# Optimization experiments

Hardware: AMD Instinct MI355X
Metric: run time of the kernel (lower is better)

Reference implementation:

```python
import jax, jax.numpy as jnp
import numpy as np

N_ATOMS = 100000
N_BONDS = 200000
MAX_NB = 6
ATOM_FDIM = 133
BOND_FDIM = 147
HIDDEN = 300
DEPTH = 3
N_MOLS = 4000


def setup_inputs() -> dict:
    key = jax.random.key(0)
    ks = jax.random.split(key, 10)
    f_atoms = jax.random.normal(ks[0], (N_ATOMS, ATOM_FDIM), dtype=jnp.float32)
    f_bonds = jax.random.normal(ks[1], (N_BONDS, BOND_FDIM), dtype=jnp.float32)
    a2b = jax.random.randint(ks[2], (N_ATOMS, MAX_NB), 0, N_BONDS, dtype=jnp.int32)
    b2a = jax.random.randint(ks[3], (N_BONDS,), 0, N_ATOMS, dtype=jnp.int32)
    b2revb = jax.random.randint(ks[4], (N_BONDS,), 0, N_BONDS, dtype=jnp.int32)
    mol_ids = jnp.sort(jax.random.randint(ks[5], (N_ATOMS,), 0, N_MOLS, dtype=jnp.int32))
    # learned params (W_i, W_h have bias=False; W_o has bias)
    sc = 0.02
    W_i = jax.random.normal(ks[6], (BOND_FDIM, HIDDEN), dtype=jnp.float32) * sc
    W_h = jax.random.normal(ks[7], (HIDDEN, HIDDEN), dtype=jnp.float32) * sc
    W_o = jax.random.normal(ks[8], (ATOM_FDIM + HIDDEN, HIDDEN), dtype=jnp.float32) * sc
    b_o = jax.random.normal(ks[9], (HIDDEN,), dtype=jnp.float32) * sc
    return {"f_atoms": f_atoms, "f_bonds": f_bonds, "a2b": a2b, "b2a": b2a,
            "b2revb": b2revb, "mol_ids": mol_ids, "W_i": W_i, "W_h": W_h,
            "W_o": W_o, "b_o": b_o}


def reference(f_atoms, f_bonds, a2b, b2a, b2revb, mol_ids, W_i, W_h, W_o, b_o):
    # input = W_i(f_bonds); message = relu(input)
    inp = f_bonds @ W_i                              # [n_bonds, H]
    message = jax.nn.relu(inp)
    for _ in range(DEPTH - 1):
        # gather incoming-bond messages per atom and sum over neighbors
        a_message = message[a2b].sum(axis=1)         # [n_atoms, H]
        # directed-bond update: m_b = sum_in(src atom) - reverse message
        message = a_message[b2a] - message[b2revb]   # [n_bonds, H]
        message = jax.nn.relu(inp + message @ W_h)   # dropout p=0 -> identity
    a_message = message[a2b].sum(axis=1)             # [n_atoms, H]
    a_input = jnp.concatenate([f_atoms, a_message], axis=1)
    atom_hiddens = jax.nn.relu(a_input @ W_o + b_o)  # [n_atoms, H]
    # per-molecule mean aggregation (a_scope loop -> segment ops)
    sums = jax.ops.segment_sum(atom_hiddens, mol_ids, num_segments=N_MOLS)
    counts = jax.ops.segment_sum(jnp.ones((atom_hiddens.shape[0], 1), atom_hiddens.dtype),
                                 mol_ids, num_segments=N_MOLS)
    # empty molecules -> cached zero vector
    return jnp.where(counts > 0, sums / jnp.maximum(counts, 1.0), 0.0)
```

## Files before the change

kernel.cpp:

```cpp
#include <hip/hip_runtime.h>

typedef unsigned short bfraw;
typedef __attribute__((ext_vector_type(8))) short short8v;
typedef __attribute__((ext_vector_type(8))) unsigned short ushort8v;
typedef __attribute__((ext_vector_type(4))) float f32x4;

static __device__ __forceinline__ float bf2f(unsigned short u) {
    union { unsigned int i; float f; } c; c.i = ((unsigned int)u) << 16; return c.f;
}
static __device__ __forceinline__ unsigned short f2bf(float f) {
    union { float f; unsigned int i; } c; c.f = f;
    unsigned int r = c.i + 0x7fffu + ((c.i >> 16) & 1u);
    return (unsigned short)(r >> 16);
}
static __device__ __forceinline__ unsigned short brelu(unsigned short u) {
    return (u & 0x8000u) ? (unsigned short)0 : u;
}
static __device__ __forceinline__ f32x4 mfma16(short8v a, short8v b, f32x4 c) {
    return __builtin_amdgcn_mfma_f32_16x16x32_bf16(a, b, c, 0, 0, 0);
}

__global__ __launch_bounds__(64) void k_pack(const float* __restrict__ W, int Krows, int row_off,
                                             bfraw* __restrict__ out) {
    const int b = blockIdx.x;
    const int ks = b / 20, ct = b - ks * 20;
    const int l = threadIdx.x;
    const int n = ct * 16 + (l & 15);
    const int kb = ks * 32 + (l >> 4) * 8;
    short8v pk;
#pragma unroll
    for (int j = 0; j < 8; ++j) {
        int k = kb + j;
        float v = (k < Krows && n < 300) ? W[(row_off + k) * 300 + n] : 0.f;
        pk[j] = (short)f2bf(v);
    }
    *(short8v*)&out[(b * 64 + l) * 8] = pk;
}


__global__ __launch_bounds__(512, 4) void k_in(const float* __restrict__ fb,
                                               const bfraw* __restrict__ Wp,
                                               bfraw* __restrict__ inp) {
    __shared__ short A[64 * 40 * 8];
    const int row0 = blockIdx.x * 64;
    const int tid = threadIdx.x;
    for (int idx = tid; idx < 64 * 20; idx += 512) {
        int r = idx / 20, c = idx - r * 20;
        const int kbase = c * 8;
        const float* src = fb + (long long)(row0 + r) * 147 + kbase;
        short8v pk;
#pragma unroll
        for (int j = 0; j < 8; ++j) {
            float v = (kbase + j < 147) ? src[j] : 0.f;
            pk[j] = (short)f2bf(v);
        }
        *(short8v*)&A[(r * 40 + (c ^ (r & 7))) * 8] = pk;
    }
    __syncthreads();
    const int w = tid >> 6, l = tid & 63;
    const int wr = w >> 2, wc = w & 3;
    const int lr = l & 15, lk = l >> 4, sw = l & 7;
    f32x4 acc[2][5];
#pragma unroll
    for (int ri = 0; ri < 2; ++ri)
#pragma unroll
        for (int i = 0; i < 5; ++i) acc[ri][i] = (f32x4){0.f, 0.f, 0.f, 0.f};
    const short8v* Ald = (const short8v*)A;
#pragma unroll
    for (int ks = 0; ks < 5; ++ks) {
        short8v bfr[2], wv[5];
#pragma unroll
        for (int ri = 0; ri < 2; ++ri)
            bfr[ri] = Ald[((wr * 2 + ri) * 16 + lr) * 40 + ((ks * 4 + lk) ^ sw)];
#pragma unroll
        for (int i = 0; i < 5; ++i)
            wv[i] = *(const short8v*)&Wp[((ks * 20 + wc * 5 + i) * 64 + l) * 8];
#pragma unroll
        for (int ri = 0; ri < 2; ++ri)
#pragma unroll
            for (int i = 0; i < 5; ++i)
                acc[ri][i] = mfma16(wv[i], bfr[ri], acc[ri][i]);
    }
    __syncthreads();
#pragma unroll
    for (int ri = 0; ri < 2; ++ri)
#pragma unroll
        for (int i = 0; i < 5; ++i) {
            const int r = (wr * 2 + ri) * 16 + lr;
            const int c16 = (wc * 5 + i) * 2 + (lk >> 1);
            ushort4 t;
            t.x = f2bf(acc[ri][i][0]); t.y = f2bf(acc[ri][i][1]);
            t.z = f2bf(acc[ri][i][2]); t.w = f2bf(acc[ri][i][3]);
            *(ushort4*)&A[(r * 40 + (c16 ^ (r & 7))) * 8 + (lk & 1) * 4] = t;
        }
    __syncthreads();
    for (int idx = tid; idx < 64 * 38; idx += 512) {
        int r = idx / 38, c = idx - r * 38;
        short8v t = *(const short8v*)&A[(r * 40 + (c ^ (r & 7))) * 8];
        *(short8v*)&inp[(long long)(row0 + r) * 304 + c * 8] = t;
    }
}

__global__ __launch_bounds__(256) void k_gather(const bfraw* __restrict__ msg,
                                                const int* __restrict__ a2b,
                                                bfraw* __restrict__ amsg) {
    int gid = blockIdx.x * 256 + threadIdx.x;
    if (gid >= 100000 * 19) return;
    int a = gid / 19, c = gid - a * 19;
    const int* nb = a2b + a * 6;
    float s0[8], s1[8];
#pragma unroll
    for (int e = 0; e < 8; ++e) { s0[e] = 0.f; s1[e] = 0.f; }
#pragma unroll
    for (int j = 0; j < 6; ++j) {
        const long long base = (long long)nb[j] * 304;
        const ushort8v v0 = *(const ushort8v*)&msg[base + c * 8];
        const ushort8v v1 = *(const ushort8v*)&msg[base + (c + 19) * 8];
#pragma unroll
        for (int e = 0; e < 8; ++e) {
            s0[e] += bf2f(brelu(v0[e]));
            s1[e] += bf2f(brelu(v1[e]));
        }
    }
    short8v o0, o1;
#pragma unroll
    for (int e = 0; e < 8; ++e) { o0[e] = (short)f2bf(s0[e]); o1[e] = (short)f2bf(s1[e]); }
    *(short8v*)&amsg[(long long)a * 304 + c * 8] = o0;
    *(short8v*)&amsg[(long long)a * 304 + (c + 19) * 8] = o1;
}

__global__ __launch_bounds__(512, 4) void k_bond(const bfraw* __restrict__ amsg,
                                                 const bfraw* __restrict__ msg,
                                                 const bfraw* __restrict__ inp,
                                                 const int* __restrict__ b2a,
                                                 const int* __restrict__ b2revb,
                                                 const bfraw* __restrict__ Wp,
                                                 bfraw* __restrict__ out) {
    __shared__ short A[64 * 40 * 8];
    const int row0 = blockIdx.x * 64;
    const int tid = threadIdx.x;
    ushort8v pf[5];
#pragma unroll
    for (int s = 0; s < 5; ++s) {
        int idx = tid + s * 512;
        if (idx < 64 * 38) {
            int r = idx / 38, c = idx - r * 38;
            pf[s] = *(const ushort8v*)&inp[(long long)(row0 + r) * 304 + c * 8];
        }
    }
#pragma unroll
    for (int it = 0; it < 5; ++it) {
        int idx = tid + it * 512;
        int r = idx / 40, c = idx - r * 40;
        short8v pk;
        if (c < 38) {
            int b = row0 + r;
            const ushort8v va = *(const ushort8v*)&amsg[(long long)b2a[b] * 304 + c * 8];
            const ushort8v vm = *(const ushort8v*)&msg[(long long)b2revb[b] * 304 + c * 8];
#pragma unroll
            for (int j = 0; j < 8; ++j)
                pk[j] = (short)f2bf(bf2f(va[j]) - bf2f(brelu(vm[j])));
        } else {
#pragma unroll
            for (int j = 0; j < 8; ++j) pk[j] = 0;
        }
        *(short8v*)&A[(r * 40 + (c ^ (r & 7))) * 8] = pk;
    }
    __syncthreads();
    const int w = tid >> 6, l = tid & 63;
    const int wr = w >> 2, wc = w & 3;
    const int lr = l & 15, lk = l >> 4, sw = l & 7;
    f32x4 acc[2][5];
#pragma unroll
    for (int ri = 0; ri < 2; ++ri)
#pragma unroll
        for (int i = 0; i < 5; ++i) acc[ri][i] = (f32x4){0.f, 0.f, 0.f, 0.f};
    const short8v* Ald = (const short8v*)A;
#pragma unroll
    for (int ks = 0; ks < 10; ++ks) {
        short8v bfr[2], wv[5];
#pragma unroll
        for (int ri = 0; ri < 2; ++ri)
            bfr[ri] = Ald[((wr * 2 + ri) * 16 + lr) * 40 + ((ks * 4 + lk) ^ sw)];
#pragma unroll
        for (int i = 0; i < 5; ++i)
            wv[i] = *(const short8v*)&Wp[((ks * 20 + wc * 5 + i) * 64 + l) * 8];
#pragma unroll
        for (int ri = 0; ri < 2; ++ri)
#pragma unroll
            for (int i = 0; i < 5; ++i)
                acc[ri][i] = mfma16(wv[i], bfr[ri], acc[ri][i]);
    }
    __syncthreads();
#pragma unroll
    for (int ri = 0; ri < 2; ++ri)
#pragma unroll
        for (int i = 0; i < 5; ++i) {
            const int r = (wr * 2 + ri) * 16 + lr;
            const int c16 = (wc * 5 + i) * 2 + (lk >> 1);
            ushort4 t;
            t.x = f2bf(acc[ri][i][0]); t.y = f2bf(acc[ri][i][1]);
            t.z = f2bf(acc[ri][i][2]); t.w = f2bf(acc[ri][i][3]);
            *(ushort4*)&A[(r * 40 + (c16 ^ (r & 7))) * 8 + (lk & 1) * 4] = t;
        }
    __syncthreads();
#pragma unroll
    for (int s = 0; s < 5; ++s) {
        int idx = tid + s * 512;
        if (idx < 64 * 38) {
            int r = idx / 38, c = idx - r * 38;
            short8v t = *(const short8v*)&A[(r * 40 + (c ^ (r & 7))) * 8];
            short8v m;
#pragma unroll
            for (int j = 0; j < 8; ++j)
                m[j] = (short)f2bf(bf2f(pf[s][j]) + bf2f((unsigned short)t[j]));
            *(short8v*)&out[(long long)(row0 + r) * 304 + c * 8] = m;
        }
    }
}

__global__ __launch_bounds__(512, 4) void k_out(const float* __restrict__ fa,
                                                const bfraw* __restrict__ msg,
                                                const int* __restrict__ a2b,
                                                const bfraw* __restrict__ WfP,
                                                const bfraw* __restrict__ WaP,
                                                const float* __restrict__ bo,
                                                bfraw* __restrict__ hid) {
    __shared__ short A[64 * 40 * 8];
    const int row0 = blockIdx.x * 64;
    const int tid = threadIdx.x;
#pragma unroll
    for (int it = 0; it < 5; ++it) {
        int idx = tid + it * 512;
        int r = idx / 40, c = idx - r * 40;
        const int row = row0 + r;
        short8v pk;
        if (c < 38 && row < 100000) {
            const int* nb = a2b + row * 6;
            float s[8];
#pragma unroll
            for (int e = 0; e < 8; ++e) s[e] = 0.f;
#pragma unroll
            for (int j = 0; j < 6; ++j) {
                const ushort8v v = *(const ushort8v*)&msg[(long long)nb[j] * 304 + c * 8];
#pragma unroll
                for (int e = 0; e < 8; ++e) s[e] += bf2f(brelu(v[e]));
            }
#pragma unroll
            for (int e = 0; e < 8; ++e) pk[e] = (short)f2bf(s[e]);
        } else {
#pragma unroll
            for (int j = 0; j < 8; ++j) pk[j] = 0;
        }
        *(short8v*)&A[(r * 40 + (c ^ (r & 7))) * 8] = pk;
    }
    __syncthreads();
    const int w = tid >> 6, l = tid & 63;
    const int wr = w >> 2, wc = w & 3;
    const int lr = l & 15, lk = l >> 4, sw = l & 7;
    f32x4 acc[2][5];
#pragma unroll
    for (int ri = 0; ri < 2; ++ri)
#pragma unroll
        for (int i = 0; i < 5; ++i) acc[ri][i] = (f32x4){0.f, 0.f, 0.f, 0.f};
    const short8v* Ald = (const short8v*)A;
#pragma unroll
    for (int ks = 0; ks < 10; ++ks) {
        short8v bfr[2], wv[5];
#pragma unroll
        for (int ri = 0; ri < 2; ++ri)
            bfr[ri] = Ald[((wr * 2 + ri) * 16 + lr) * 40 + ((ks * 4 + lk) ^ sw)];
#pragma unroll
        for (int i = 0; i < 5; ++i)
            wv[i] = *(const short8v*)&WaP[((ks * 20 + wc * 5 + i) * 64 + l) * 8];
#pragma unroll
        for (int ri = 0; ri < 2; ++ri)
#pragma unroll
            for (int i = 0; i < 5; ++i)
                acc[ri][i] = mfma16(wv[i], bfr[ri], acc[ri][i]);
    }
    __syncthreads();
    for (int idx = tid; idx < 64 * 20; idx += 512) {
        int r = idx / 20, c = idx - r * 20;
        const int row = row0 + r;
        const int kbase = c * 8;
        short8v pk;
        if (row < 100000) {
            const float* src = fa + (long long)row * 133 + kbase;
#pragma unroll
            for (int j = 0; j < 8; ++j) {
                float v = (kbase + j < 133) ? src[j] : 0.f;
                pk[j] = (short)f2bf(v);
            }
        } else {
#pragma unroll
            for (int j = 0; j < 8; ++j) pk[j] = 0;
        }
        *(short8v*)&A[(r * 40 + (c ^ (r & 7))) * 8] = pk;
    }
    __syncthreads();
#pragma unroll
    for (int ks = 0; ks < 5; ++ks) {
        short8v bfr[2], wv[5];
#pragma unroll
        for (int ri = 0; ri < 2; ++ri)
            bfr[ri] = Ald[((wr * 2 + ri) * 16 + lr) * 40 + ((ks * 4 + lk) ^ sw)];
#pragma unroll
        for (int i = 0; i < 5; ++i)
            wv[i] = *(const short8v*)&WfP[((ks * 20 + wc * 5 + i) * 64 + l) * 8];
#pragma unroll
        for (int ri = 0; ri < 2; ++ri)
#pragma unroll
            for (int i = 0; i < 5; ++i)
                acc[ri][i] = mfma16(wv[i], bfr[ri], acc[ri][i]);
    }
    __syncthreads();
#pragma unroll
    for (int ri = 0; ri < 2; ++ri)
#pragma unroll
        for (int i = 0; i < 5; ++i) {
            const int r = (wr * 2 + ri) * 16 + lr;
            const int c16 = (wc * 5 + i) * 2 + (lk >> 1);
            ushort4 t;
            t.x = f2bf(acc[ri][i][0]); t.y = f2bf(acc[ri][i][1]);
            t.z = f2bf(acc[ri][i][2]); t.w = f2bf(acc[ri][i][3]);
            *(ushort4*)&A[(r * 40 + (c16 ^ (r & 7))) * 8 + (lk & 1) * 4] = t;
        }
    __syncthreads();
    for (int idx = tid; idx < 64 * 38; idx += 512) {
        int r = idx / 38, c = idx - r * 38;
        const int row = row0 + r;
        if (row >= 100000) continue;
        short8v t = *(const short8v*)&A[(r * 40 + (c ^ (r & 7))) * 8];
        float4 b0 = *(const float4*)&bo[c * 8];
        float4 b1 = (c < 37) ? *(const float4*)&bo[c * 8 + 4]
                             : make_float4(0.f, 0.f, 0.f, 0.f);
        float bias[8] = {b0.x, b0.y, b0.z, b0.w, b1.x, b1.y, b1.z, b1.w};
        short8v m;
#pragma unroll
        for (int j = 0; j < 8; ++j)
            m[j] = (short)f2bf(fmaxf(bf2f((unsigned short)t[j]) + bias[j], 0.f));
        *(short8v*)&hid[(long long)row * 304 + c * 8] = m;
    }
}

__global__ __launch_bounds__(320) void k_mean(const bfraw* __restrict__ hid,
                                              const int* __restrict__ mol,
                                              float* __restrict__ out) {
    __shared__ float red[8][304];
    const int m = blockIdx.x;
    const int natoms = 100000;
    int lo = 0, hi = natoms;
    while (lo < hi) { int mid = (lo + hi) >> 1; if (mol[mid] < m) lo = mid + 1; else hi = mid; }
    const int start = lo;
    lo = start; hi = natoms;
    while (lo < hi) { int mid = (lo + hi) >> 1; if (mol[mid] <= m) lo = mid + 1; else hi = mid; }
    const int end = lo;
    const int tid = threadIdx.x;
    const int p = tid / 38, c = tid - p * 38;
    if (tid < 304) {
        float s[8];
#pragma unroll
        for (int e = 0; e < 8; ++e) s[e] = 0.f;
        for (int a = start + p; a < end; a += 8) {
            const ushort8v v = *(const ushort8v*)&hid[(long long)a * 304 + c * 8];
#pragma unroll
            for (int e = 0; e < 8; ++e) s[e] += bf2f(v[e]);
        }
#pragma unroll
        for (int e = 0; e < 8; ++e) red[p][c * 8 + e] = s[e];
    }
    __syncthreads();
    if (tid < 300) {
        float t = 0.f;
#pragma unroll
        for (int p2 = 0; p2 < 8; ++p2) t += red[p2][tid];
        const int n = end - start;
        out[m * 300 + tid] = (n > 0) ? (t / (float)n) : 0.f;
    }
}

extern "C" void kernel_launch(void* const* d_in, const int* in_sizes, int n_in,
                              void* d_out, int out_size, void* d_ws, size_t ws_size,
                              hipStream_t stream) {
    const float* f_atoms = (const float*)d_in[0];
    const float* f_bonds = (const float*)d_in[1];
    const int* a2b      = (const int*)d_in[2];
    const int* b2a      = (const int*)d_in[3];
    const int* b2revb   = (const int*)d_in[4];
    const int* mol_ids  = (const int*)d_in[5];
    const float* W_i    = (const float*)d_in[6];
    const float* W_h    = (const float*)d_in[7];
    const float* W_o    = (const float*)d_in[8];
    const float* b_o    = (const float*)d_in[9];
    float* out = (float*)d_out;

    char* wsb = (char*)d_ws;
    bfraw* inp  = (bfraw*)(wsb);
    bfraw* M1   = (bfraw*)(wsb + 121600000ll);
    bfraw* M2   = (bfraw*)(wsb + 243200000ll);
    bfraw* amsg = (bfraw*)(wsb + 364800000ll);
    bfraw* WiP   = (bfraw*)(wsb + 425600000ll);
    bfraw* WhP   = (bfraw*)(wsb + 425702400ll);
    bfraw* WoFaP = (bfraw*)(wsb + 425907200ll);
    bfraw* WoAmP = (bfraw*)(wsb + 426009600ll);

    k_pack<<<100, 64, 0, stream>>>(W_i, 147, 0, WiP);
    k_pack<<<200, 64, 0, stream>>>(W_h, 300, 0, WhP);
    k_pack<<<100, 64, 0, stream>>>(W_o, 133, 0, WoFaP);
    k_pack<<<200, 64, 0, stream>>>(W_o, 300, 133, WoAmP);

    const int nb_blocks = 200000 / 64;
    const int na_blocks = (100000 + 63) / 64;
    const int gather_blocks = (100000 * 19 + 255) / 256;

    k_in<<<nb_blocks, 512, 0, stream>>>(f_bonds, WiP, inp);

    k_gather<<<gather_blocks, 256, 0, stream>>>(inp, a2b, amsg);
    k_bond<<<nb_blocks, 512, 0, stream>>>(amsg, inp, inp, b2a, b2revb, WhP, M1);
    k_gather<<<gather_blocks, 256, 0, stream>>>(M1, a2b, amsg);
    k_bond<<<nb_blocks, 512, 0, stream>>>(amsg, M1, inp, b2a, b2revb, WhP, M2);

    bfraw* hid = M1;
    k_out<<<na_blocks, 512, 0, stream>>>(f_atoms, M2, a2b, WoFaP, WoAmP, b_o, hid);
    k_mean<<<4000, 320, 0, stream>>>(hid, mol_ids, out);
}
```

Measured before the change: 675.1 us.

## Fuse atom neighbor gather into bond update kernel and vectorize input load

Removes the separate k_gather kernel and its amsg buffer. Each bond row now recomputes the sum over the six a2b neighbor messages of its source atom directly inside k_bond, which trades the write and reread of the atom-message array for redundant neighbor gathers, roughly twice as many since there are two bonds per atom. The bond-feature staging in k_in also switches to coalesced float4 loads with scattered bf16 LDS writes, and pad columns are zeroed separately. Reading six random neighbor rows per bond may make k_bond more bound on memory latency.

```diff
diff --git a/kernel.cpp b/kernel.cpp
--- a/kernel.cpp
+++ b/kernel.cpp
@@ -44,17 +44,28 @@
     __shared__ short A[64 * 40 * 8];
     const int row0 = blockIdx.x * 64;
     const int tid = threadIdx.x;
-    for (int idx = tid; idx < 64 * 20; idx += 512) {
-        int r = idx / 20, c = idx - r * 20;
-        const int kbase = c * 8;
-        const float* src = fb + (long long)(row0 + r) * 147 + kbase;
-        short8v pk;
-#pragma unroll
-        for (int j = 0; j < 8; ++j) {
-            float v = (kbase + j < 147) ? src[j] : 0.f;
-            pk[j] = (short)f2bf(v);
-        }
-        *(short8v*)&A[(r * 40 + (c ^ (r & 7))) * 8] = pk;
+    if (tid < 128) {
+        int r = tid >> 1, c = 18 + (tid & 1);
+        short8v z = {0, 0, 0, 0, 0, 0, 0, 0};
+        *(short8v*)&A[(r * 40 + (c ^ (r & 7))) * 8] = z;
+    }
+    __syncthreads();
+    const float4* fb4 = (const float4*)(fb + (long long)row0 * 147);
+#pragma unroll 1
+    for (int s = 0; s < 5; ++s) {
+        int idx = tid + s * 512;
+        if (idx < 2352) {
+            float4 v = fb4[idx];
+            const float* ve = (const float*)&v;
+            int k0 = idx * 4;
+#pragma unroll
+            for (int e = 0; e < 4; ++e) {
+                int k = k0 + e;
+                int r = k / 147;
+                int c = k - r * 147;
+                A[(r * 40 + ((c >> 3) ^ (r & 7))) * 8 + (c & 7)] = (short)f2bf(ve[e]);
+            }
+        }
     }
     __syncthreads();
     const int w = tid >> 6, l = tid & 63;
@@ -101,37 +112,9 @@
     }
 }
 
-__global__ __launch_bounds__(256) void k_gather(const bfraw* __restrict__ msg,
-                                                const int* __restrict__ a2b,
-                                                bfraw* __restrict__ amsg) {
-    int gid = blockIdx.x * 256 + threadIdx.x;
-    if (gid >= 100000 * 19) return;
-    int a = gid / 19, c = gid - a * 19;
-    const int* nb = a2b + a * 6;
-    float s0[8], s1[8];
-#pragma unroll
-    for (int e = 0; e < 8; ++e) { s0[e] = 0.f; s1[e] = 0.f; }
-#pragma unroll
-    for (int j = 0; j < 6; ++j) {
-        const long long base = (long long)nb[j] * 304;
-        const ushort8v v0 = *(const ushort8v*)&msg[base + c * 8];
-        const ushort8v v1 = *(const ushort8v*)&msg[base + (c + 19) * 8];
-#pragma unroll
-        for (int e = 0; e < 8; ++e) {
-            s0[e] += bf2f(brelu(v0[e]));
-            s1[e] += bf2f(brelu(v1[e]));
-        }
-    }
-    short8v o0, o1;
-#pragma unroll
-    for (int e = 0; e < 8; ++e) { o0[e] = (short)f2bf(s0[e]); o1[e] = (short)f2bf(s1[e]); }
-    *(short8v*)&amsg[(long long)a * 304 + c * 8] = o0;
-    *(short8v*)&amsg[(long long)a * 304 + (c + 19) * 8] = o1;
-}
-
-__global__ __launch_bounds__(512, 4) void k_bond(const bfraw* __restrict__ amsg,
-                                                 const bfraw* __restrict__ msg,
+__global__ __launch_bounds__(512, 4) void k_bond(const bfraw* __restrict__ msg,
                                                  const bfraw* __restrict__ inp,
+                                                 const int* __restrict__ a2b,
                                                  const int* __restrict__ b2a,
                                                  const int* __restrict__ b2revb,
                                                  const bfraw* __restrict__ Wp,
@@ -139,6 +122,11 @@
     __shared__ short A[64 * 40 * 8];
     const int row0 = blockIdx.x * 64;
     const int tid = threadIdx.x;
+    if (tid < 128) {
+        int r = tid >> 1, c = 38 + (tid & 1);
+        short8v z = {0, 0, 0, 0, 0, 0, 0, 0};
+        *(short8v*)&A[(r * 40 + (c ^ (r & 7))) * 8] = z;
+    }
     ushort8v pf[5];
 #pragma unroll
     for (int s = 0; s < 5; ++s) {
@@ -148,23 +136,30 @@
             pf[s] = *(const ushort8v*)&inp[(long long)(row0 + r) * 304 + c * 8];
         }
     }
-#pragma unroll
-    for (int it = 0; it < 5; ++it) {
-        int idx = tid + it * 512;
-        int r = idx / 40, c = idx - r * 40;
-        short8v pk;
-        if (c < 38) {
-            int b = row0 + r;
-            const ushort8v va = *(const ushort8v*)&amsg[(long long)b2a[b] * 304 + c * 8];
-            const ushort8v vm = *(const ushort8v*)&msg[(long long)b2revb[b] * 304 + c * 8];
-#pragma unroll
-            for (int j = 0; j < 8; ++j)
-                pk[j] = (short)f2bf(bf2f(va[j]) - bf2f(brelu(vm[j])));
-        } else {
-#pragma unroll
-            for (int j = 0; j < 8; ++j) pk[j] = 0;
-        }
-        *(short8v*)&A[(r * 40 + (c ^ (r & 7))) * 8] = pk;
+#pragma unroll 1
+    for (int s = 0; s < 5; ++s) {
+        int idx = tid + s * 512;
+        if (idx < 64 * 38) {
+            int r = idx / 38, c = idx - r * 38;
+            const int b = row0 + r;
+            const int a = b2a[b];
+            const int rv = b2revb[b];
+            const int* nb = a2b + a * 6;
+            float s8[8];
+            const ushort8v vm = *(const ushort8v*)&msg[(long long)rv * 304 + c * 8];
+#pragma unroll
+            for (int e = 0; e < 8; ++e) s8[e] = -bf2f(brelu(vm[e]));
+#pragma unroll
+            for (int j = 0; j < 6; ++j) {
+                const ushort8v v = *(const ushort8v*)&msg[(long long)nb[j] * 304 + c * 8];
+#pragma unroll
+                for (int e = 0; e < 8; ++e) s8[e] += bf2f(brelu(v[e]));
+            }
+            short8v pk;
+#pragma unroll
+            for (int e = 0; e < 8; ++e) pk[e] = (short)f2bf(s8[e]);
+            *(short8v*)&A[(r * 40 + (c ^ (r & 7))) * 8] = pk;
+        }
     }
     __syncthreads();
     const int w = tid >> 6, l = tid & 63;
@@ -399,7 +394,6 @@
     bfraw* inp  = (bfraw*)(wsb);
     bfraw* M1   = (bfraw*)(wsb + 121600000ll);
     bfraw* M2   = (bfraw*)(wsb + 243200000ll);
-    bfraw* amsg = (bfraw*)(wsb + 364800000ll);
     bfraw* WiP   = (bfraw*)(wsb + 425600000ll);
     bfraw* WhP   = (bfraw*)(wsb + 425702400ll);
     bfraw* WoFaP = (bfraw*)(wsb + 425907200ll);
@@ -412,14 +406,10 @@
 
     const int nb_blocks = 200000 / 64;
     const int na_blocks = (100000 + 63) / 64;
-    const int gather_blocks = (100000 * 19 + 255) / 256;
 
     k_in<<<nb_blocks, 512, 0, stream>>>(f_bonds, WiP, inp);
-
-    k_gather<<<gather_blocks, 256, 0, stream>>>(inp, a2b, amsg);
-    k_bond<<<nb_blocks, 512, 0, stream>>>(amsg, inp, inp, b2a, b2revb, WhP, M1);
-    k_gather<<<gather_blocks, 256, 0, stream>>>(M1, a2b, amsg);
-    k_bond<<<nb_blocks, 512, 0, stream>>>(amsg, M1, inp, b2a, b2revb, WhP, M2);
+    k_bond<<<nb_blocks, 512, 0, stream>>>(inp, inp, a2b, b2a, b2revb, WhP, M1);
+    k_bond<<<nb_blocks, 512, 0, stream>>>(M1, inp, a2b, b2a, b2revb, WhP, M2);
 
     bfraw* hid = M1;
     k_out<<<na_blocks, 512, 0, stream>>>(f_atoms, M2, a2b, WoFaP, WoAmP, b_o, hid);
```

New measurement: 688.2 us. About the same (+1.9%).
